# Optimization experiments

Measured on AMD Instinct MI355X. Metric: run time of the kernel, lower is better.

The kernel has to match this reference:

```python
import jax, jax.numpy as jnp
import numpy as np

SOS = 1

def setup_inputs() -> dict:
    key = jax.random.key(0)
    ks = jax.random.split(key, 12)
    B, S, T, H, V = 64, 128, 32, 1024, 32000
    sc = 0.02
    return {
        'encoder_outputs': jax.random.normal(ks[0], (B, S, H), jnp.float32),
        'encoder_hidden': jax.random.normal(ks[1], (1, B, H), jnp.float32),
        'target_tensor': jax.random.randint(ks[2], (B, T), 0, V),
        'embedding': jax.random.normal(ks[3], (V, H), jnp.float32) * sc,
        'Wa': jax.random.normal(ks[4], (H, H), jnp.float32) * sc,
        'ba': jnp.zeros((H,), jnp.float32),
        'Ua': jax.random.normal(ks[5], (H, H), jnp.float32) * sc,
        'bu': jnp.zeros((H,), jnp.float32),
        'Va': jax.random.normal(ks[6], (1, H), jnp.float32) * sc,
        'bv': jnp.zeros((1,), jnp.float32),
        'W_ih': jax.random.normal(ks[7], (3 * H, 2 * H), jnp.float32) * sc,
        'b_ih': jnp.zeros((3 * H,), jnp.float32),
        'W_hh': jax.random.normal(ks[8], (3 * H, H), jnp.float32) * sc,
        'b_hh': jnp.zeros((3 * H,), jnp.float32),
        'W_out': jax.random.normal(ks[9], (V, H), jnp.float32) * sc,
        'b_out': jnp.zeros((V,), jnp.float32),
    }

def reference(encoder_outputs, encoder_hidden, target_tensor, embedding,
              Wa, ba, Ua, bu, Va, bv, W_ih, b_ih, W_hh, b_hh, W_out, b_out):
    B, S, H = encoder_outputs.shape
    T = target_tensor.shape[1]
    # teacher forcing: input at step i is SOS for i=0 else target[:, i-1]
    tokens = jnp.concatenate([jnp.full((B, 1), SOS, target_tensor.dtype),
                              target_tensor[:, :-1]], axis=1)  # (B,T)
    emb = embedding[tokens]  # (B,T,H); dropout is identity (eval)
    keys_proj = jnp.einsum('bsh,gh->bsg', encoder_outputs, Ua) + bu  # Ua(keys), (B,S,H)
    h0 = encoder_hidden[0]  # (B,H)

    def step(h, x_t):
        # Bahdanau attention: Va(tanh(Wa q + Ua k))
        q = h @ Wa.T + ba  # (B,H)
        scores = jnp.einsum('bsh,h->bs', jnp.tanh(q[:, None, :] + keys_proj), Va[0]) + bv[0]
        w = jax.nn.softmax(scores, axis=-1)  # (B,S)
        ctx = jnp.einsum('bs,bsh->bh', w, encoder_outputs)
        x = jnp.concatenate([x_t, ctx], axis=-1)  # (B,2H)
        # GRU cell (PyTorch convention)
        gi = x @ W_ih.T + b_ih
        gh = h @ W_hh.T + b_hh
        ir, iz, inn = jnp.split(gi, 3, axis=-1)
        hr, hz, hn = jnp.split(gh, 3, axis=-1)
        r = jax.nn.sigmoid(ir + hr)
        z = jax.nn.sigmoid(iz + hz)
        n = jnp.tanh(inn + r * hn)
        h_new = (1.0 - z) * n + z * h
        logits = h_new @ W_out.T + b_out  # (B,V)
        return h_new, (logits, w)

    h_final, (logits, weights) = jax.lax.scan(step, h0, jnp.swapaxes(emb, 0, 1))
    log_probs = jax.nn.log_softmax(jnp.swapaxes(logits, 0, 1), axis=-1)  # (B,T,V)
    attentions = jnp.swapaxes(weights, 0, 1)  # (B,T,S)
    return log_probs, h_final[None], attentions
```

## Files before the change

### kernel.cpp

```cpp
#include <hip/hip_runtime.h>


typedef unsigned short u16;
typedef __bf16 bf16x8 __attribute__((ext_vector_type(8)));
typedef float f32x4 __attribute__((ext_vector_type(4)));
typedef u16 u16x8 __attribute__((ext_vector_type(8)));

#define DEV __device__ __forceinline__

DEV u16 f2b(float f) {
  union { float f; unsigned u; } v; v.f = f;
  unsigned r = v.u + 0x7fffu + ((v.u >> 16) & 1u);
  return (u16)(r >> 16);
}
DEV float b2f(u16 b) {
  union { unsigned u; float f; } v; v.u = ((unsigned)b) << 16;
  return v.f;
}
DEV float sigm(float x) { return 1.f / (1.f + __expf(-x)); }
DEV float ftanh(float x) {
  x = fminf(fmaxf(x, -20.f), 20.f);
  float e = __expf(2.f * x);
  return (e - 1.f) / (e + 1.f);
}
DEV void gl16(const void* g, void* l) {
  __builtin_amdgcn_global_load_lds((const __attribute__((address_space(1))) void*)g,
                                   (__attribute__((address_space(3))) void*)l, 16, 0, 0);
}

__global__ __launch_bounds__(256) void prepk(const float* __restrict__ enc, const float* __restrict__ Ua,
                                             const float* __restrict__ Wa, const float* __restrict__ Whh,
                                             const float* __restrict__ Wout, const float* __restrict__ Wih,
                                             const float* __restrict__ embd, const int* __restrict__ tgt,
                                             const float* __restrict__ eh, u16* __restrict__ enc_b,
                                             u16* __restrict__ Ua_b, u16* __restrict__ Wa_b,
                                             u16* __restrict__ Whh_b, u16* __restrict__ Wout_b,
                                             u16* __restrict__ Wih1_b, u16* __restrict__ Wih2_b,
                                             u16* __restrict__ emb_b, float* __restrict__ hf,
                                             u16* __restrict__ hb0) {
  const long q0 = 2097152;
  const long q1 = q0 + 262144;
  const long q2 = q1 + 262144;
  const long q3 = q2 + 786432;
  const long q4 = q3 + 8192000;
  const long q5 = q4 + 1572864;
  const long q6 = q5 + 524288;
  const long q7 = q6 + 16384;
  long stride = (long)gridDim.x * 256;
  for (long i = (long)blockIdx.x * 256 + threadIdx.x; i < q7; i += stride) {
    if (i < q4) {
      const float* src; u16* dst; long off;
      if (i < q0) { src = enc; dst = enc_b; off = i; }
      else if (i < q1) { src = Ua; dst = Ua_b; off = i - q0; }
      else if (i < q2) { src = Wa; dst = Wa_b; off = i - q1; }
      else if (i < q3) { src = Whh; dst = Whh_b; off = i - q2; }
      else { src = Wout; dst = Wout_b; off = i - q3; }
      float4 v = ((const float4*)src)[off];
      ushort4 o; o.x = f2b(v.x); o.y = f2b(v.y); o.z = f2b(v.z); o.w = f2b(v.w);
      ((ushort4*)dst)[off] = o;
    } else if (i < q5) {
      long off = i - q4;
      long e = off * 4;
      int row = (int)(e >> 11), col = (int)(e & 2047);
      float4 v = ((const float4*)Wih)[off];
      ushort4 o; o.x = f2b(v.x); o.y = f2b(v.y); o.z = f2b(v.z); o.w = f2b(v.w);
      u16* dst = (col < 1024) ? (Wih1_b + (size_t)row * 1024 + col)
                              : (Wih2_b + (size_t)row * 1024 + col - 1024);
      *(ushort4*)dst = o;
    } else if (i < q6) {
      long off = i - q5;
      size_t e = (size_t)off * 4;
      int h = (int)(e & 1023);
      int bt = (int)(e >> 10);
      int b = bt >> 5, t = bt & 31;
      int tok = (t == 0) ? 1 : tgt[b * 32 + t - 1];
      const float* src = embd + (size_t)tok * 1024 + h;
      float4 v = *(const float4*)src;
      ushort4 o; o.x = f2b(v.x); o.y = f2b(v.y); o.z = f2b(v.z); o.w = f2b(v.w);
      *(ushort4*)(emb_b + e) = o;
    } else {
      long off = i - q6;
      float4 v = ((const float4*)eh)[off];
      ((float4*)hf)[off] = v;
      ushort4 o; o.x = f2b(v.x); o.y = f2b(v.y); o.z = f2b(v.z); o.w = f2b(v.w);
      ((ushort4*)hb0)[off] = o;
    }
  }
}

template <int MODE>
__global__ __launch_bounds__(256) void gemm_tile(const u16* __restrict__ A, const u16* __restrict__ Bm,
                                                 const float* __restrict__ bias, float* __restrict__ Cf,
                                                 u16* __restrict__ Cb, int K, int ldc, int nTM) {
  __shared__ __attribute__((aligned(16))) u16 As[128 * 32];
  __shared__ __attribute__((aligned(16))) u16 Bs[128 * 32];
  const int tid = threadIdx.x, lane = tid & 63, w = tid >> 6;
  const int chunk = gridDim.x >> 3, wg = blockIdx.x;
  const int id = (wg & 7) * chunk + (wg >> 3);
  const int m = id % nTM, n = id / nTM;
  const int m0 = m * 128, n0 = n * 128;
  const int wm = w >> 1, wn = w & 1;
  const int l16 = lane & 15, kg = lane >> 4;
  const int srow = lane >> 2;
  const int skk = (((lane & 3) ^ ((srow >> 1) & 3)) * 8);
  const int slot = (kg ^ ((l16 >> 1) & 3)) * 8;

  f32x4 acc[4][4];
#pragma unroll
  for (int i = 0; i < 4; ++i)
#pragma unroll
    for (int j = 0; j < 4; ++j) acc[i][j] = f32x4{0.f, 0.f, 0.f, 0.f};

  for (int k0 = 0; k0 < K; k0 += 32) {
#pragma unroll
    for (int ch = 0; ch < 2; ++ch) {
      int c = w + ch * 4;
      gl16(A + (size_t)(m0 + c * 16 + srow) * K + k0 + skk, &As[c * 512]);
      gl16(Bm + (size_t)(n0 + c * 16 + srow) * K + k0 + skk, &Bs[c * 512]);
    }
    __syncthreads();
    bf16x8 av[4], bv[4];
#pragma unroll
    for (int i = 0; i < 4; ++i) av[i] = *(const bf16x8*)&As[(wm * 4 + i) * 512 + l16 * 32 + slot];
#pragma unroll
    for (int j = 0; j < 4; ++j) bv[j] = *(const bf16x8*)&Bs[(wn * 4 + j) * 512 + l16 * 32 + slot];
#pragma unroll
    for (int i = 0; i < 4; ++i)
#pragma unroll
      for (int j = 0; j < 4; ++j)
        acc[i][j] = __builtin_amdgcn_mfma_f32_16x16x32_bf16(av[i], bv[j], acc[i][j], 0, 0, 0);
    __syncthreads();
  }
#pragma unroll
  for (int i = 0; i < 4; ++i) {
    int rowb = m0 + (wm * 4 + i) * 16 + kg * 4;
#pragma unroll
    for (int j = 0; j < 4; ++j) {
      int col = n0 + (wn * 4 + j) * 16 + l16;
      float bb = (MODE == 2) ? 0.f : bias[col];
#pragma unroll
      for (int r = 0; r < 4; ++r) {
        int row = rowb + r;
        float v = acc[i][j][r] + bb;
        if (MODE == 0) Cf[(size_t)row * ldc + col] = v;
        else Cb[(size_t)row * ldc + col] = f2b(v);
      }
    }
  }
}

template <int MODE>
__global__ __launch_bounds__(256, 2) void gemm_wide(const u16* __restrict__ A, const u16* __restrict__ Bm,
                                                    const float* __restrict__ bias, float* __restrict__ Cf,
                                                    u16* __restrict__ Cb, int K, int ldc) {
  __shared__ __attribute__((aligned(16))) u16 As[128 * 64];
  __shared__ __attribute__((aligned(16))) u16 Bs[256 * 64];
  const int tid = threadIdx.x, lane = tid & 63, w = tid >> 6;
  const int chunk = gridDim.x >> 3, wg = blockIdx.x;
  const int id = (wg & 7) * chunk + (wg >> 3);
  const int r_ = id % 80;
  const int m = r_ & 15, n = 5 * (id / 80) + (r_ >> 4);
  const int m0 = m * 128, n0 = n * 256;
  const int wm = w >> 1, wn = w & 1;
  const int l16 = lane & 15, kg = lane >> 4;
  const int srow = lane >> 2;
  const int skk = (((lane & 3) ^ ((srow >> 1) & 3)) * 8);
  const int slot = (kg ^ ((l16 >> 1) & 3)) * 8;

  f32x4 acc[4][8];
#pragma unroll
  for (int i = 0; i < 4; ++i)
#pragma unroll
    for (int j = 0; j < 8; ++j) acc[i][j] = f32x4{0.f, 0.f, 0.f, 0.f};

  for (int k0 = 0; k0 < K; k0 += 64) {
#pragma unroll
    for (int ch = 0; ch < 2; ++ch) {
      int c = w + ch * 4;
#pragma unroll
      for (int p = 0; p < 2; ++p)
        gl16(A + (size_t)(m0 + c * 16 + srow) * K + k0 + p * 32 + skk, &As[c * 1024 + p * 512]);
    }
#pragma unroll
    for (int ch = 0; ch < 4; ++ch) {
      int c = w + ch * 4;
#pragma unroll
      for (int p = 0; p < 2; ++p)
        gl16(Bm + (size_t)(n0 + c * 16 + srow) * K + k0 + p * 32 + skk, &Bs[c * 1024 + p * 512]);
    }
    __syncthreads();
#pragma unroll
    for (int p = 0; p < 2; ++p) {
      bf16x8 av[4], bv[8];
#pragma unroll
      for (int i = 0; i < 4; ++i)
        av[i] = *(const bf16x8*)&As[(wm * 4 + i) * 1024 + p * 512 + l16 * 32 + slot];
#pragma unroll
      for (int j = 0; j < 8; ++j)
        bv[j] = *(const bf16x8*)&Bs[(wn * 8 + j) * 1024 + p * 512 + l16 * 32 + slot];
#pragma unroll
      for (int i = 0; i < 4; ++i)
#pragma unroll
        for (int j = 0; j < 8; ++j)
          acc[i][j] = __builtin_amdgcn_mfma_f32_16x16x32_bf16(av[i], bv[j], acc[i][j], 0, 0, 0);
    }
    __syncthreads();
  }
#pragma unroll
  for (int i = 0; i < 4; ++i) {
    int rowb = m0 + (wm * 4 + i) * 16 + kg * 4;
#pragma unroll
    for (int j = 0; j < 8; ++j) {
      int col = n0 + (wn * 8 + j) * 16 + l16;
      float bb = bias[col];
#pragma unroll
      for (int r = 0; r < 4; ++r) {
        int row = rowb + r;
        float v = acc[i][j][r] + bb;
        int b_ = row & 63, t_ = row >> 6;
        size_t ro = ((size_t)b_ * 32 + t_) * ldc + col;
        if (MODE == 0) Cf[ro] = v; else Cb[ro] = f2b(v);
      }
    }
  }
}

__global__ __launch_bounds__(256) void qkghk(const u16* __restrict__ hb, const u16* __restrict__ W1,
                                             float* __restrict__ qghp) {
  const int tid = threadIdx.x, lane = tid & 63, w = tid >> 6;
  const int l16 = lane & 15, kg = lane >> 4;
  const int pg = blockIdx.x >> 2, ks = blockIdx.x & 3;
  const u16* ap = hb + (size_t)(w * 16 + l16) * 1024 + ks * 256 + kg * 8;
  const u16* bp = W1 + (size_t)(pg * 16 + l16) * 1024 + ks * 256 + kg * 8;
  f32x4 a = {0.f, 0.f, 0.f, 0.f};
#pragma unroll
  for (int k0 = 0; k0 < 256; k0 += 32)
    a = __builtin_amdgcn_mfma_f32_16x16x32_bf16(*(const bf16x8*)(ap + k0), *(const bf16x8*)(bp + k0),
                                                a, 0, 0, 0);
  const int col = pg * 16 + l16;
#pragma unroll
  for (int r = 0; r < 4; ++r) {
    int b = w * 16 + kg * 4 + r;
    qghp[(size_t)ks * 262144 + b * 4096 + col] = a[r];
  }
}

__global__ __launch_bounds__(256) void scorekq(const float* __restrict__ qghp, const float* __restrict__ ba,
                                               const float* __restrict__ Va, const u16* __restrict__ kp,
                                               float* __restrict__ sc) {
  const int b = blockIdx.x >> 3, s8 = blockIdx.x & 7;
  const int tid = threadIdx.x, lane = tid & 63, w = tid >> 6;
  __shared__ float qs[1024], vas[1024];
#pragma unroll
  for (int j = 0; j < 4; ++j) {
    int e = tid + j * 256;
    qs[e] = qghp[b * 4096 + e] + qghp[262144 + b * 4096 + e] + qghp[524288 + b * 4096 + e] +
            qghp[786432 + b * 4096 + e] + ba[e];
    vas[e] = Va[e];
  }
  __syncthreads();
#pragma unroll
  for (int si = 0; si < 4; ++si) {
    int s = s8 * 16 + w * 4 + si;
    const bf16x8* kv = (const bf16x8*)(kp + ((size_t)b * 128 + s) * 1024);
    float a = 0.f;
#pragma unroll
    for (int i2 = 0; i2 < 2; ++i2) {
      int e = lane + 64 * i2;
      bf16x8 k8 = kv[e];
#pragma unroll
      for (int j = 0; j < 8; ++j) a += vas[e * 8 + j] * ftanh(qs[e * 8 + j] + (float)k8[j]);
    }
#pragma unroll
    for (int off = 32; off; off >>= 1) a += __shfl_xor(a, off);
    if (lane == 0) sc[b * 128 + s] = a;
  }
}

__global__ __launch_bounds__(512) void wsumgate(const float* __restrict__ scb, const u16* __restrict__ encW2,
                                                const float* __restrict__ gie, const float* __restrict__ qghp,
                                                const float* __restrict__ bhh, float* __restrict__ hf,
                                                u16* __restrict__ hbW, u16* __restrict__ hall,
                                                float* __restrict__ hfin, float* __restrict__ att_out, int t) {
  const int b = blockIdx.x >> 2, cg = blockIdx.x & 3;
  const int tid = threadIdx.x, lane = tid & 63, w = tid >> 6;
  __shared__ float wsm[128];
  __shared__ float pa[3][2][256];
  if (w == 0) {
    float v0 = scb[b * 128 + lane], v1 = scb[b * 128 + 64 + lane];
    float mx = fmaxf(v0, v1);
#pragma unroll
    for (int off = 32; off; off >>= 1) mx = fmaxf(mx, __shfl_xor(mx, off));
    float e0 = __expf(v0 - mx), e1 = __expf(v1 - mx);
    float sm = e0 + e1;
#pragma unroll
    for (int off = 32; off; off >>= 1) sm += __shfl_xor(sm, off);
    float inv = 1.f / sm;
    e0 *= inv; e1 *= inv;
    wsm[lane] = e0; wsm[lane + 64] = e1;
    if (cg == 0) {
      size_t ao = ((size_t)b * 32 + t) * 128;
      att_out[ao + lane] = e0;
      att_out[ao + lane + 64] = e1;
    }
  }
  __syncthreads();
  const int ct = tid & 255, half = tid >> 8;
  const int col = cg * 256 + ct;
  float a0 = 0.f, a1 = 0.f, a2 = 0.f;
  const u16* ep = encW2 + (size_t)b * 128 * 3072 + (size_t)half * 64 * 3072 + col;
#pragma unroll 8
  for (int s = 0; s < 64; ++s) {
    float ws = wsm[half * 64 + s];
    a0 += ws * b2f(ep[0]);
    a1 += ws * b2f(ep[1024]);
    a2 += ws * b2f(ep[2048]);
    ep += 3072;
  }
  pa[0][half][ct] = a0; pa[1][half][ct] = a1; pa[2][half][ct] = a2;
  __syncthreads();
  if (tid < 256) {
    float g0 = pa[0][0][tid] + pa[0][1][tid];
    float g1 = pa[1][0][tid] + pa[1][1][tid];
    float g2 = pa[2][0][tid] + pa[2][1][tid];
    const int c2 = cg * 256 + tid;
    const float* ge = gie + ((size_t)b * 32 + t) * 3072 + c2;
    const float* qg = qghp + (size_t)b * 4096 + 1024 + c2;
    float hr = qg[0] + qg[262144] + qg[524288] + qg[786432] + bhh[c2];
    float hz = qg[1024] + qg[1024 + 262144] + qg[1024 + 524288] + qg[1024 + 786432] + bhh[c2 + 1024];
    float hn = qg[2048] + qg[2048 + 262144] + qg[2048 + 524288] + qg[2048 + 786432] + bhh[c2 + 2048];
    float rr = sigm(g0 + ge[0] + hr);
    float zz = sigm(g1 + ge[1024] + hz);
    float nn = ftanh(g2 + ge[2048] + rr * hn);
    const int i = b * 1024 + c2;
    float hp = hf[i];
    float hv = (1.f - zz) * nn + zz * hp;
    hf[i] = hv;
    u16 h16 = f2b(hv);
    hbW[i] = h16;
    hall[((size_t)t * 64 + b) * 1024 + c2] = h16;
    if (t == 31) hfin[i] = hv;
  }
}

__global__ __launch_bounds__(256) void smaxctxk(const float* __restrict__ sc, const u16* __restrict__ encb,
                                                u16* __restrict__ ctxb, float* __restrict__ att_out, int t) {
  const int b = blockIdx.x >> 2, hq = blockIdx.x & 3;
  const int tid = threadIdx.x, lane = tid & 63, w = tid >> 6;
  __shared__ float wsm[128];
  if (w == 0) {
    float v0 = sc[b * 128 + lane], v1 = sc[b * 128 + 64 + lane];
    float mx = fmaxf(v0, v1);
#pragma unroll
    for (int off = 32; off; off >>= 1) mx = fmaxf(mx, __shfl_xor(mx, off));
    float e0 = __expf(v0 - mx), e1 = __expf(v1 - mx);
    float sm = e0 + e1;
#pragma unroll
    for (int off = 32; off; off >>= 1) sm += __shfl_xor(sm, off);
    float inv = 1.f / sm;
    e0 *= inv; e1 *= inv;
    wsm[lane] = e0; wsm[lane + 64] = e1;
    if (hq == 0) {
      size_t ao = ((size_t)b * 32 + t) * 128;
      att_out[ao + lane] = e0;
      att_out[ao + lane + 64] = e1;
    }
  }
  __syncthreads();
  const int h = hq * 256 + tid;
  const u16* ep = encb + (size_t)b * 131072 + h;
  float c = 0.f;
#pragma unroll 8
  for (int s = 0; s < 128; ++s) c += wsm[s] * b2f(ep[(size_t)s * 1024]);
  ctxb[(size_t)b * 1024 + h] = f2b(c);
}

__global__ __launch_bounds__(256) void gi2w(const u16* __restrict__ ctxb, const u16* __restrict__ Wih2,
                                            float* __restrict__ gic) {
  const int tid = threadIdx.x, lane = tid & 63, w = tid >> 6;
  const int l16 = lane & 15, kg = lane >> 4;
  const int c0 = blockIdx.x * 16;
  const u16* ap = ctxb + (size_t)(w * 16 + l16) * 1024 + kg * 8;
  const u16* bp = Wih2 + (size_t)(c0 + l16) * 1024 + kg * 8;
  f32x4 a0 = {0.f, 0.f, 0.f, 0.f}, a1 = {0.f, 0.f, 0.f, 0.f};
#pragma unroll 4
  for (int k0 = 0; k0 < 1024; k0 += 64) {
    a0 = __builtin_amdgcn_mfma_f32_16x16x32_bf16(*(const bf16x8*)(ap + k0), *(const bf16x8*)(bp + k0),
                                                 a0, 0, 0, 0);
    a1 = __builtin_amdgcn_mfma_f32_16x16x32_bf16(*(const bf16x8*)(ap + k0 + 32),
                                                 *(const bf16x8*)(bp + k0 + 32), a1, 0, 0, 0);
  }
  const int col = c0 + l16;
#pragma unroll
  for (int r = 0; r < 4; ++r) {
    int b = w * 16 + kg * 4 + r;
    gic[(size_t)b * 3072 + col] = a0[r] + a1[r];
  }
}

__global__ __launch_bounds__(256) void gatesq(const float* __restrict__ gic, const float* __restrict__ gie,
                                              const float* __restrict__ qghp, const float* __restrict__ bhh,
                                              float* __restrict__ hf, u16* __restrict__ hbW,
                                              u16* __restrict__ hall, float* __restrict__ hfin, int t) {
  const int i = blockIdx.x * 256 + threadIdx.x;
  const int b = i >> 10, col = i & 1023;
  const float* gi = gic + (size_t)b * 3072 + col;
  const float* ge = gie + ((size_t)b * 32 + t) * 3072 + col;
  const float* qg = qghp + (size_t)b * 4096 + 1024 + col;
  float hr = qg[0] + qg[262144] + qg[524288] + qg[786432] + bhh[col];
  float hz = qg[1024] + qg[1024 + 262144] + qg[1024 + 524288] + qg[1024 + 786432] + bhh[col + 1024];
  float hn = qg[2048] + qg[2048 + 262144] + qg[2048 + 524288] + qg[2048 + 786432] + bhh[col + 2048];
  float rr = sigm(gi[0] + ge[0] + hr);
  float zz = sigm(gi[1024] + ge[1024] + hz);
  float nn = ftanh(gi[2048] + ge[2048] + rr * hn);
  float hp = hf[i];
  float hv = (1.f - zz) * nn + zz * hp;
  hf[i] = hv;
  u16 h16 = f2b(hv);
  hbW[i] = h16;
  hall[((size_t)t * 64 + b) * 1024 + col] = h16;
  if (t == 31) hfin[i] = hv;
}

__global__ __launch_bounds__(256) void logsoftk(const u16* __restrict__ lg, float* __restrict__ out) {
  const int row = blockIdx.x, tid = threadIdx.x, lane = tid & 63, w = tid >> 6;
  const u16x8* p = (const u16x8*)(lg + (size_t)row * 32000);
  __shared__ float red[4];
  u16x8 d[16];
#pragma unroll
  for (int j = 0; j < 16; ++j) {
    int i = tid + j * 256;
    if (i < 4000) d[j] = p[i];
  }
  float mx = -3.0e38f;
#pragma unroll
  for (int j = 0; j < 16; ++j) {
    int i = tid + j * 256;
    if (i < 4000)
#pragma unroll
      for (int k = 0; k < 8; ++k) mx = fmaxf(mx, b2f(d[j][k]));
  }
#pragma unroll
  for (int off = 32; off; off >>= 1) mx = fmaxf(mx, __shfl_xor(mx, off));
  if (lane == 0) red[w] = mx;
  __syncthreads();
  mx = fmaxf(fmaxf(red[0], red[1]), fmaxf(red[2], red[3]));
  __syncthreads();
  float s = 0.f;
#pragma unroll
  for (int j = 0; j < 16; ++j) {
    int i = tid + j * 256;
    if (i < 4000)
#pragma unroll
      for (int k = 0; k < 8; ++k) s += __expf(b2f(d[j][k]) - mx);
  }
#pragma unroll
  for (int off = 32; off; off >>= 1) s += __shfl_xor(s, off);
  if (lane == 0) red[w] = s;
  __syncthreads();
  float c = mx + __logf(red[0] + red[1] + red[2] + red[3]);
  float* op = out + (size_t)row * 32000;
#pragma unroll
  for (int j = 0; j < 16; ++j) {
    int i = tid + j * 256;
    if (i < 4000) {
      f32x4 o0, o1;
#pragma unroll
      for (int k = 0; k < 4; ++k) { o0[k] = b2f(d[j][k]) - c; o1[k] = b2f(d[j][k + 4]) - c; }
      *(f32x4*)(op + i * 8) = o0;
      *(f32x4*)(op + i * 8 + 4) = o1;
    }
  }
}

__global__ __launch_bounds__(256) void rowstatk(const float* __restrict__ lp, float* __restrict__ c) {
  int row = blockIdx.x;
  const float4* p = (const float4*)(lp + (size_t)row * 32000);
  int tid = threadIdx.x, lane = tid & 63, w = tid >> 6;
  __shared__ float redm[4], reds[4];
  float mx = -3.0e38f;
  for (int i = tid; i < 8000; i += 256) {
    float4 v = p[i];
    mx = fmaxf(mx, fmaxf(fmaxf(v.x, v.y), fmaxf(v.z, v.w)));
  }
#pragma unroll
  for (int off = 32; off; off >>= 1) mx = fmaxf(mx, __shfl_xor(mx, off));
  if (lane == 0) redm[w] = mx;
  __syncthreads();
  mx = fmaxf(fmaxf(redm[0], redm[1]), fmaxf(redm[2], redm[3]));
  float s = 0.f;
  for (int i = tid; i < 8000; i += 256) {
    float4 v = p[i];
    s += __expf(v.x - mx) + __expf(v.y - mx) + __expf(v.z - mx) + __expf(v.w - mx);
  }
#pragma unroll
  for (int off = 32; off; off >>= 1) s += __shfl_xor(s, off);
  if (lane == 0) reds[w] = s;
  __syncthreads();
  if (tid == 0) c[row] = mx + __logf(reds[0] + reds[1] + reds[2] + reds[3]);
}

__global__ __launch_bounds__(256) void subk(float* __restrict__ lp, const float* __restrict__ c) {
  const long n4 = (long)64 * 32 * 32000 / 4;
  long stride = (long)gridDim.x * 256;
  for (long i = (long)blockIdx.x * 256 + threadIdx.x; i < n4; i += stride) {
    float4 v = ((float4*)lp)[i];
    float cc = c[i / 8000];
    v.x -= cc; v.y -= cc; v.z -= cc; v.w -= cc;
    ((float4*)lp)[i] = v;
  }
}

extern "C" void kernel_launch(void* const* d_in, const int* in_sizes, int n_in, void* d_out, int out_size,
                              void* d_ws, size_t ws_size, hipStream_t stream) {
  (void)in_sizes; (void)n_in; (void)out_size;
  constexpr int B = 64, S = 128, T = 32, H = 1024, V = 32000;

  const float* enc  = (const float*)d_in[0];
  const float* ehid = (const float*)d_in[1];
  const int*   tgt  = (const int*)d_in[2];
  const float* embd = (const float*)d_in[3];
  const float* Wa   = (const float*)d_in[4];
  const float* ba   = (const float*)d_in[5];
  const float* Ua   = (const float*)d_in[6];
  const float* bu   = (const float*)d_in[7];
  const float* Va   = (const float*)d_in[8];
  const float* Wih  = (const float*)d_in[10];
  const float* bih  = (const float*)d_in[11];
  const float* Whh  = (const float*)d_in[12];
  const float* bhh  = (const float*)d_in[13];
  const float* Wout = (const float*)d_in[14];
  const float* bout = (const float*)d_in[15];

  char* wp = (char*)d_ws;
  auto alloc = [&](size_t bytes) {
    char* p = wp;
    wp += (bytes + 255) & ~(size_t)255;
    return p;
  };
  u16* enc_b  = (u16*)alloc((size_t)B * S * H * 2);
  u16* kp_b   = (u16*)alloc((size_t)B * S * H * 2);
  u16* Ua_b   = (u16*)alloc((size_t)H * H * 2);
  u16* W1_b   = (u16*)alloc((size_t)4096 * 1024 * 2);
  u16* Wih1_b = (u16*)alloc((size_t)3072 * 1024 * 2);
  u16* Wih2_b = (u16*)alloc((size_t)3072 * 1024 * 2);
  u16* Wout_b = (u16*)alloc((size_t)V * H * 2);
  u16* emb_b  = (u16*)alloc((size_t)B * T * H * 2);
  u16* hall_b = (u16*)alloc((size_t)T * B * H * 2);
  float* gie  = (float*)alloc((size_t)B * T * 3072 * 4);
  float* qghp = (float*)alloc((size_t)4 * B * 4096 * 4);
  float* scb  = (float*)alloc((size_t)B * S * 4);
  float* gic  = (float*)alloc((size_t)B * 3072 * 4);
  u16* ctx_b  = (u16*)alloc((size_t)B * H * 2);
  u16* hb0    = (u16*)alloc((size_t)B * H * 2);
  u16* hb1    = (u16*)alloc((size_t)B * H * 2);
  float* h_f  = (float*)alloc((size_t)B * H * 4);
  float* rowc = (float*)alloc(2048 * 4);
  size_t base_need = (size_t)(wp - (char*)d_ws);
  u16* encW2 = (u16*)alloc((size_t)B * S * 3072 * 2);
  bool have_w2 = ((size_t)(wp - (char*)d_ws) <= ws_size);
  u16* lg_b = (u16*)alloc((size_t)B * T * V * 2);
  bool bflog = ((size_t)(wp - (char*)d_ws) <= ws_size);
  if (base_need > ws_size) return;

  float* out_lp = (float*)d_out;
  float* out_hf = out_lp + (size_t)B * T * V;
  float* out_at = out_hf + (size_t)B * H;

  u16* Wa_slot = W1_b;
  u16* Whh_slot = W1_b + (size_t)1024 * 1024;
  prepk<<<2048, 256, 0, stream>>>(enc, Ua, Wa, Whh, Wout, Wih, embd, tgt, ehid,
                                  enc_b, Ua_b, Wa_slot, Whh_slot, Wout_b,
                                  Wih1_b, Wih2_b, emb_b, h_f, hb0);

  gemm_tile<1><<<512, 256, 0, stream>>>(enc_b, Ua_b, bu, nullptr, kp_b, H, H, 64);
  gemm_tile<0><<<384, 256, 0, stream>>>(emb_b, Wih1_b, bih, gie, nullptr, H, 3072, 16);
  if (have_w2) {
    gemm_tile<2><<<1536, 256, 0, stream>>>(enc_b, Wih2_b, nullptr, nullptr, encW2, H, 3072, 64);
  }

  for (int t = 0; t < T; ++t) {
    u16* hbR = (t & 1) ? hb1 : hb0;
    u16* hbW = (t & 1) ? hb0 : hb1;
    qkghk<<<1024, 256, 0, stream>>>(hbR, W1_b, qghp);
    scorekq<<<512, 256, 0, stream>>>(qghp, ba, Va, kp_b, scb);
    if (have_w2) {
      wsumgate<<<256, 512, 0, stream>>>(scb, encW2, gie, qghp, bhh, h_f, hbW, hall_b,
                                        out_hf, out_at, t);
    } else {
      smaxctxk<<<256, 256, 0, stream>>>(scb, enc_b, ctx_b, out_at, t);
      gi2w<<<192, 256, 0, stream>>>(ctx_b, Wih2_b, gic);
      gatesq<<<256, 256, 0, stream>>>(gic, gie, qghp, bhh, h_f, hbW, hall_b, out_hf, t);
    }
  }

  if (bflog) {
    gemm_wide<1><<<2000, 256, 0, stream>>>(hall_b, Wout_b, bout, nullptr, lg_b, H, V);
    logsoftk<<<2048, 256, 0, stream>>>(lg_b, out_lp);
  } else {
    gemm_wide<0><<<2000, 256, 0, stream>>>(hall_b, Wout_b, bout, out_lp, nullptr, H, V);
    rowstatk<<<2048, 256, 0, stream>>>(out_lp, rowc);
    subk<<<2048, 256, 0, stream>>>(out_lp, rowc);
  }
}
```

Measured before the change: 1.409 ms.

## Use wide GEMM for encoder-Wih2 projection and vectorize per-step context-gate reduction

The one-time encoder×W_ih(context part) projection now runs on the larger 128x256 gemm_wide kernel with a simple row-major tile map, replacing the smaller gemm_tile launch. Inside the per-step wsumgate kernel, each thread now loads 8 contiguous bf16 values per row with vector loads over 8 sequence positions. The 16 partial sums per column are then reduced through a larger shared buffer. This is meant to cut per-step memory instruction count on the 32 serial timesteps. The cost is more shared memory and registers per block.

```diff
diff --git a/kernel.cpp b/kernel.cpp
--- a/kernel.cpp
+++ b/kernel.cpp
@@ -149,17 +149,18 @@
   }
 }
 
-template <int MODE>
+template <int MODE, int MAP>
 __global__ __launch_bounds__(256, 2) void gemm_wide(const u16* __restrict__ A, const u16* __restrict__ Bm,
                                                     const float* __restrict__ bias, float* __restrict__ Cf,
-                                                    u16* __restrict__ Cb, int K, int ldc) {
+                                                    u16* __restrict__ Cb, int K, int ldc, int nTM) {
   __shared__ __attribute__((aligned(16))) u16 As[128 * 64];
   __shared__ __attribute__((aligned(16))) u16 Bs[256 * 64];
   const int tid = threadIdx.x, lane = tid & 63, w = tid >> 6;
   const int chunk = gridDim.x >> 3, wg = blockIdx.x;
   const int id = (wg & 7) * chunk + (wg >> 3);
-  const int r_ = id % 80;
-  const int m = r_ & 15, n = 5 * (id / 80) + (r_ >> 4);
+  int m, n;
+  if (MAP == 0) { int r_ = id % 80; m = r_ & 15; n = 5 * (id / 80) + (r_ >> 4); }
+  else { m = id % nTM; n = id / nTM; }
   const int m0 = m * 128, n0 = n * 256;
   const int wm = w >> 1, wn = w & 1;
   const int l16 = lane & 15, kg = lane >> 4;
@@ -212,14 +213,18 @@
 #pragma unroll
     for (int j = 0; j < 8; ++j) {
       int col = n0 + (wn * 8 + j) * 16 + l16;
-      float bb = bias[col];
+      float bb = (MODE == 2) ? 0.f : bias[col];
 #pragma unroll
       for (int r = 0; r < 4; ++r) {
         int row = rowb + r;
         float v = acc[i][j][r] + bb;
-        int b_ = row & 63, t_ = row >> 6;
-        size_t ro = ((size_t)b_ * 32 + t_) * ldc + col;
-        if (MODE == 0) Cf[ro] = v; else Cb[ro] = f2b(v);
+        if (MODE == 2) {
+          Cb[(size_t)row * ldc + col] = f2b(v);
+        } else {
+          int b_ = row & 63, t_ = row >> 6;
+          size_t ro = ((size_t)b_ * 32 + t_) * ldc + col;
+          if (MODE == 0) Cf[ro] = v; else Cb[ro] = f2b(v);
+        }
       }
     }
   }
@@ -285,7 +290,7 @@
   const int b = blockIdx.x >> 2, cg = blockIdx.x & 3;
   const int tid = threadIdx.x, lane = tid & 63, w = tid >> 6;
   __shared__ float wsm[128];
-  __shared__ float pa[3][2][256];
+  __shared__ float pa[16][3][256];
   if (w == 0) {
     float v0 = scb[b * 128 + lane], v1 = scb[b * 128 + 64 + lane];
     float mx = fmaxf(v0, v1);
@@ -305,24 +310,41 @@
     }
   }
   __syncthreads();
-  const int ct = tid & 255, half = tid >> 8;
-  const int col = cg * 256 + ct;
-  float a0 = 0.f, a1 = 0.f, a2 = 0.f;
-  const u16* ep = encW2 + (size_t)b * 128 * 3072 + (size_t)half * 64 * 3072 + col;
-#pragma unroll 8
-  for (int s = 0; s < 64; ++s) {
-    float ws = wsm[half * 64 + s];
-    a0 += ws * b2f(ep[0]);
-    a1 += ws * b2f(ep[1024]);
-    a2 += ws * b2f(ep[2048]);
+  const int cg8 = tid & 31, sg = tid >> 5;
+  const int colBase = cg * 256 + cg8 * 8;
+  float a0[8], a1[8], a2[8];
+#pragma unroll
+  for (int k = 0; k < 8; ++k) { a0[k] = 0.f; a1[k] = 0.f; a2[k] = 0.f; }
+  const u16* ep = encW2 + ((size_t)b * 128 + sg * 8) * 3072 + colBase;
+#pragma unroll
+  for (int si = 0; si < 8; ++si) {
+    float ws = wsm[sg * 8 + si];
+    u16x8 v0 = *(const u16x8*)(ep);
+    u16x8 v1 = *(const u16x8*)(ep + 1024);
+    u16x8 v2 = *(const u16x8*)(ep + 2048);
+#pragma unroll
+    for (int k = 0; k < 8; ++k) {
+      a0[k] += ws * b2f(v0[k]);
+      a1[k] += ws * b2f(v1[k]);
+      a2[k] += ws * b2f(v2[k]);
+    }
     ep += 3072;
   }
-  pa[0][half][ct] = a0; pa[1][half][ct] = a1; pa[2][half][ct] = a2;
+  {
+    f32x4 t0 = {a0[0], a0[1], a0[2], a0[3]}, t1 = {a0[4], a0[5], a0[6], a0[7]};
+    *(f32x4*)&pa[sg][0][cg8 * 8] = t0; *(f32x4*)&pa[sg][0][cg8 * 8 + 4] = t1;
+    f32x4 t2 = {a1[0], a1[1], a1[2], a1[3]}, t3 = {a1[4], a1[5], a1[6], a1[7]};
+    *(f32x4*)&pa[sg][1][cg8 * 8] = t2; *(f32x4*)&pa[sg][1][cg8 * 8 + 4] = t3;
+    f32x4 t4 = {a2[0], a2[1], a2[2], a2[3]}, t5 = {a2[4], a2[5], a2[6], a2[7]};
+    *(f32x4*)&pa[sg][2][cg8 * 8] = t4; *(f32x4*)&pa[sg][2][cg8 * 8 + 4] = t5;
+  }
   __syncthreads();
   if (tid < 256) {
-    float g0 = pa[0][0][tid] + pa[0][1][tid];
-    float g1 = pa[1][0][tid] + pa[1][1][tid];
-    float g2 = pa[2][0][tid] + pa[2][1][tid];
+    float g0 = 0.f, g1 = 0.f, g2 = 0.f;
+#pragma unroll
+    for (int s2 = 0; s2 < 16; ++s2) {
+      g0 += pa[s2][0][tid]; g1 += pa[s2][1][tid]; g2 += pa[s2][2][tid];
+    }
     const int c2 = cg * 256 + tid;
     const float* ge = gie + ((size_t)b * 32 + t) * 3072 + c2;
     const float* qg = qghp + (size_t)b * 4096 + 1024 + c2;
@@ -576,7 +598,7 @@
   gemm_tile<1><<<512, 256, 0, stream>>>(enc_b, Ua_b, bu, nullptr, kp_b, H, H, 64);
   gemm_tile<0><<<384, 256, 0, stream>>>(emb_b, Wih1_b, bih, gie, nullptr, H, 3072, 16);
   if (have_w2) {
-    gemm_tile<2><<<1536, 256, 0, stream>>>(enc_b, Wih2_b, nullptr, nullptr, encW2, H, 3072, 64);
+    gemm_wide<2, 1><<<768, 256, 0, stream>>>(enc_b, Wih2_b, nullptr, nullptr, encW2, H, 3072, 64);
   }
 
   for (int t = 0; t < T; ++t) {
@@ -595,10 +617,10 @@
   }
 
   if (bflog) {
-    gemm_wide<1><<<2000, 256, 0, stream>>>(hall_b, Wout_b, bout, nullptr, lg_b, H, V);
+    gemm_wide<1, 0><<<2000, 256, 0, stream>>>(hall_b, Wout_b, bout, nullptr, lg_b, H, V, 16);
     logsoftk<<<2048, 256, 0, stream>>>(lg_b, out_lp);
   } else {
-    gemm_wide<0><<<2000, 256, 0, stream>>>(hall_b, Wout_b, bout, out_lp, nullptr, H, V);
+    gemm_wide<0, 0><<<2000, 256, 0, stream>>>(hall_b, Wout_b, bout, out_lp, nullptr, H, V, 16);
     rowstatk<<<2048, 256, 0, stream>>>(out_lp, rowc);
     subk<<<2048, 256, 0, stream>>>(out_lp, rowc);
   }
```

After: 1.420 ms. Within noise of the previous version (+0.8%).
